# Kernel optimization log

Hardware: AMD Instinct MI355X
Metric: run time of the kernel (lower is better)

The kernel has to match this reference:

```python
import math
import jax, jax.numpy as jnp
import numpy as np

B, DIM, C, N = 1024, 512, 1000, 8
R = 0.05
WEIGHT_LAMBDA = 0.3
CN = C * N
TOPK = math.ceil(R * CN)  # 400


def setup_inputs() -> dict:
    key = jax.random.key(0)
    k1, k2, k3 = jax.random.split(key, 3)
    x = jax.random.normal(k1, (B, DIM), dtype=jnp.float32)
    # kaiming_uniform_(a=sqrt(5)) on a (DIM, CN) tensor: fan_in = CN (torch 2D fan_in = size(1)),
    # gain = sqrt(2/(1+a^2)) = sqrt(1/3), bound = gain * sqrt(3/fan_in)
    bound = math.sqrt(1.0 / 3.0) * math.sqrt(3.0 / CN)
    proxies = jax.random.uniform(k2, (DIM, CN), dtype=jnp.float32, minval=-bound, maxval=bound)
    target = jax.random.randint(k3, (B,), 0, C)
    return {"x": x, "proxies": proxies, "target": target}


def reference(x, proxies, target):
    instance_label = jnp.repeat(jnp.arange(C), N)  # (CN,)

    # F.normalize(Proxies, p=2, dim=0) with eps=1e-12 clamp
    norm = jnp.maximum(jnp.linalg.norm(proxies, axis=0, keepdims=True), 1e-12)
    centers = proxies / norm  # (DIM, CN)

    similarity = x @ centers  # (B, CN)

    positive_mask = (target[:, None] == instance_label[None, :]).astype(similarity.dtype)

    # topk over similarity boosted so all positives are included, then scatter 1s
    _, idx = jax.lax.top_k(similarity + 1000.0 * positive_mask, TOPK)  # (B, TOPK)
    mask = jnp.zeros_like(similarity).at[jnp.arange(B)[:, None], idx].set(1.0)
    mask = jax.lax.stop_gradient(mask)

    prob_a = mask * similarity  # (B, CN)
    # matmul with block one-hot y_instance_onehot == sum over the N proxies of each class
    logits = prob_a.reshape(B, C, N).sum(axis=-1)  # (B, C)

    logits_mask = jax.lax.stop_gradient((logits != 0.0).astype(logits.dtype))
    exp_l = jnp.exp(logits) * logits_mask
    predict = exp_l / (1e-8 + exp_l.sum(axis=1, keepdims=True))

    # sum(-y_onehot * log(predict+1e-20), 1) == -log(predict[b, target[b]] + 1e-20)
    loss_classify = jnp.mean(-jnp.log(predict[jnp.arange(B), target] + 1e-20))

    # regularizer: (centers.T @ centers) @ y_instance_onehot, fused as
    # centers.T @ (per-class sum of centers) -- identical math, avoids the CNxCN matrix
    centers_cls = centers.reshape(DIM, C, N).sum(axis=-1)  # (DIM, C)
    centers_logits = centers.T @ centers_cls  # (CN, C)
    logp = jax.nn.log_softmax(centers_logits, axis=1)
    reg = -jnp.mean(logp[jnp.arange(CN), instance_label])

    total = loss_classify + WEIGHT_LAMBDA * reg
    return (total, loss_classify)
```

## Files before the change

### kernel.cpp

```cpp
#include <hip/hip_runtime.h>
#include <hip/hip_bf16.h>
#include <math.h>

#define PB   1024
#define PDIM 512
#define PC   1000
#define PN   8
#define PCN  8000
#define PTOPK 400
#define NONPOS_K 392
#define NBIN 1024
#define CANDMAX 1024

typedef __bf16 bf16x8 __attribute__((ext_vector_type(8)));
typedef __bf16 bf16x4 __attribute__((ext_vector_type(4)));
typedef float  f32x4  __attribute__((ext_vector_type(4)));

__device__ static inline void async_load16(const __bf16* g, __bf16* l) {
    __builtin_amdgcn_global_load_lds(
        (const __attribute__((address_space(1))) void*)g,
        (__attribute__((address_space(3))) void*)l,
        16, 0, 0);
}

__global__ __launch_bounds__(256) void k_pre(const float* __restrict__ x,
                                             const float* __restrict__ P,
                                             __bf16* __restrict__ xb,
                                             float* __restrict__ ssqp,
                                             float* __restrict__ esd,
                                             float* __restrict__ padf,
                                             float* __restrict__ acc) {
    int b = blockIdx.x, tid = threadIdx.x;
    if (b == 0 && tid < 8) acc[tid] = 0.f;
    if (b < 512) {
        int i = b * 256 + tid;
        float4 v = ((const float4*)x)[i];
        bf16x4 o;
        o[0] = (__bf16)v.x; o[1] = (__bf16)v.y; o[2] = (__bf16)v.z; o[3] = (__bf16)v.w;
        ((bf16x4*)xb)[i] = o;
    } else if (b < 768) {
        int idx = b - 512;
        int slice = idx & 7, jb = idx >> 3;
        int j = jb * 256 + tid;
        if (j < PCN) {
            const float* p = P + (size_t)(slice * 64) * PCN + j;
            float ss = 0.f;
#pragma unroll 8
            for (int r = 0; r < 64; ++r) {
                float v = p[(size_t)r * PCN];
                ss = fmaf(v, v, ss);
            }
            ssqp[slice * PCN + j] = ss;
        }
    } else {
        int i = (b - 768) * 256 + tid;
        if (i < 16000) esd[i] = 0.f;
        else if (i < 16000 + 6144) padf[i - 16000] = 0.f;
    }
}

__global__ __launch_bounds__(256) void k_tpose(const float* __restrict__ P,
                                               const float* __restrict__ ssqp,
                                               __bf16* __restrict__ Pt,
                                               __bf16* __restrict__ ccls) {
    __shared__ float t[64][65];
    __shared__ float sinv[64];
    int tid = threadIdx.x;
    int tx = tid & 63, ty = tid >> 6;
    int j0 = blockIdx.x * 64, d0 = blockIdx.y * 64;
    if (tid < 64) {
        float sq = 0.f;
#pragma unroll
        for (int p2 = 0; p2 < 8; ++p2) sq += ssqp[p2 * PCN + j0 + tid];
        sinv[tid] = 1.0f / fmaxf(sqrtf(sq), 1e-12f);
    }
#pragma unroll
    for (int r = 0; r < 16; ++r) {
        int d = d0 + ty * 16 + r;
        t[ty * 16 + r][tx] = P[(size_t)d * PCN + j0 + tx];
    }
    __syncthreads();
    float cs0 = 0.f, cs1 = 0.f;
#pragma unroll
    for (int r = 0; r < 16; ++r) {
        int jl = ty * 16 + r;
        float val = t[tx][jl] * sinv[jl];
        Pt[(size_t)(j0 + jl) * PDIM + d0 + tx] = (__bf16)val;
        if (r < 8) cs0 += val; else cs1 += val;
    }
    int c0 = (j0 >> 3) + ty * 2;
    ccls[(size_t)c0 * PDIM + d0 + tx] = (__bf16)cs0;
    ccls[(size_t)(c0 + 1) * PDIM + d0 + tx] = (__bf16)cs1;
}

#define GEMM_STAGE(A, Bt, Ma, Nb, m0, n0, buf, k0) {                          \
    _Pragma("unroll")                                                         \
    for (int pass = 0; pass < 2; ++pass) {                                    \
        int cc_ = pass * 256 + w * 64 + lane;                                 \
        int arow = (m0) + (cc_ >> 2); if (arow > (Ma) - 1) arow = (Ma) - 1;   \
        async_load16((A) + (size_t)arow * PDIM + (k0) + (cc_ & 3) * 8,        \
                     &As[buf][cc_ * 8]);                                      \
        int brow = (n0) + (cc_ >> 2); if (brow > (Nb) - 1) brow = (Nb) - 1;   \
        async_load16((Bt) + (size_t)brow * PDIM + (k0) + (cc_ & 3) * 8,       \
                     &Bs[buf][cc_ * 8]);                                      \
    } }

#define GEMM_CORE(A, Bt, Ma, Nb, m0, n0)                                      \
    GEMM_STAGE(A, Bt, Ma, Nb, m0, n0, 0, 0)                                   \
    for (int it = 0; it < 16; ++it) {                                         \
        int cur = it & 1;                                                     \
        __syncthreads();                                                      \
        if (it < 15) GEMM_STAGE(A, Bt, Ma, Nb, m0, n0, cur ^ 1, (it + 1) * 32)\
        bf16x8 av[4], bv[4];                                                  \
        _Pragma("unroll")                                                     \
        for (int i = 0; i < 4; ++i) {                                         \
            av[i] = *(const bf16x8*)&As[cur][(wr * 64 + i * 16 + l15) * 32 + quad * 8]; \
            bv[i] = *(const bf16x8*)&Bs[cur][(wc * 64 + i * 16 + l15) * 32 + quad * 8]; \
        }                                                                     \
        _Pragma("unroll")                                                     \
        for (int i = 0; i < 4; ++i)                                           \
            _Pragma("unroll")                                                 \
            for (int j = 0; j < 4; ++j)                                       \
                acc[i][j] = __builtin_amdgcn_mfma_f32_16x16x32_bf16(          \
                    av[i], bv[j], acc[i][j], 0, 0, 0);                        \
    }

__global__ __launch_bounds__(256) void k_gemms(const __bf16* __restrict__ xb,
                                               const __bf16* __restrict__ Pt,
                                               const __bf16* __restrict__ ccls,
                                               __bf16* __restrict__ simb,
                                               float* __restrict__ esum,
                                               float* __restrict__ diag) {
    __shared__ __bf16 As[2][128 * 32];
    __shared__ __bf16 Bs[2][128 * 32];
    int tid = threadIdx.x;
    int w = tid >> 6, lane = tid & 63;
    int wr = w >> 1, wc = w & 1;
    int quad = lane >> 4, l15 = lane & 15;
    f32x4 acc[4][4] = {};
    int id = blockIdx.x;
    if (id < 504) {
        int n0 = (id % 63) * 128, m0 = (id / 63) * 128;
        GEMM_CORE(xb, Pt, PB, PCN, m0, n0)
#pragma unroll
        for (int i = 0; i < 4; ++i) {
            int r0 = m0 + wr * 64 + i * 16 + quad * 4;
#pragma unroll
            for (int j = 0; j < 4; ++j) {
                int cc = n0 + wc * 64 + j * 16 + l15;
                if (cc < PCN) {
#pragma unroll
                    for (int r = 0; r < 4; ++r)
                        simb[(size_t)(r0 + r) * PCN + cc] = (__bf16)acc[i][j][r];
                }
            }
        }
    } else {
        int id2 = id - 504;
        int n0 = (id2 % 8) * 128, m0 = (id2 / 8) * 128;
        GEMM_CORE(Pt, ccls, PCN, PB, m0, n0)
#pragma unroll
        for (int i = 0; i < 4; ++i) {
            int r0 = m0 + wr * 64 + i * 16 + quad * 4;
            float psum[4] = {0.f, 0.f, 0.f, 0.f};
#pragma unroll
            for (int j = 0; j < 4; ++j) {
                int cc = n0 + wc * 64 + j * 16 + l15;
                bool cvalid = (cc < PC);
#pragma unroll
                for (int r = 0; r < 4; ++r) {
                    float v = acc[i][j][r];
                    psum[r] += cvalid ? expf(v) : 0.f;
                    int rr = r0 + r;
                    if (cvalid && rr < PCN && cc == (rr >> 3)) diag[rr] = v;
                }
            }
#pragma unroll
            for (int off = 1; off < 16; off <<= 1)
#pragma unroll
                for (int r = 0; r < 4; ++r)
                    psum[r] += __shfl_xor(psum[r], off, 64);
            if (l15 == 0) {
#pragma unroll
                for (int r = 0; r < 4; ++r) {
                    int rr = r0 + r;
                    if (rr < PCN) atomicAdd(&esum[rr], psum[r]);
                }
            }
        }
    }
}

__global__ __launch_bounds__(256) void k_rowloss(const __bf16* __restrict__ sim,
                                                 const int* __restrict__ target,
                                                 float* __restrict__ acc) {
    __shared__ unsigned hist[NBIN];
    __shared__ float redf[8];
    __shared__ unsigned wtot[4];
    __shared__ float cand[CANDMAX];
    __shared__ unsigned candn;
    __shared__ int s_bin, s_A;
    __shared__ float s_tau;
    __shared__ int s_gt, s_eq;
    __shared__ float s_et;

    int b = blockIdx.x, tid = threadIdx.x;
    int lane = tid & 63, wv = tid >> 6;
    const bf16x8* row8 = (const bf16x8*)(sim + (size_t)b * PCN);
    int targ = target[b];

#pragma unroll
    for (int k = 0; k < 4; ++k) hist[tid + 256 * k] = 0u;
    if (tid == 0) candn = 0u;

    float pv[4][8];
    float lmn = INFINITY, lmx = -INFINITY;
#pragma unroll
    for (int k = 0; k < 4; ++k) {
        int c = tid + 256 * k;
        if (c < PC) {
            bf16x8 vv = row8[c];
#pragma unroll
            for (int n = 0; n < 8; ++n) pv[k][n] = (float)vv[n];
            if (c != targ) {
#pragma unroll
                for (int n = 0; n < 8; ++n) {
                    lmn = fminf(lmn, pv[k][n]);
                    lmx = fmaxf(lmx, pv[k][n]);
                }
            }
        } else {
#pragma unroll
            for (int n = 0; n < 8; ++n) pv[k][n] = 0.f;
        }
    }
    for (int off = 32; off; off >>= 1) {
        lmn = fminf(lmn, __shfl_down(lmn, off, 64));
        lmx = fmaxf(lmx, __shfl_down(lmx, off, 64));
    }
    if (lane == 0) { redf[wv] = lmn; redf[4 + wv] = lmx; }
    __syncthreads();
    float lo = fminf(fminf(redf[0], redf[1]), fminf(redf[2], redf[3]));
    float hi = fmaxf(fmaxf(redf[4], redf[5]), fmaxf(redf[6], redf[7]));
    float range = hi - lo;
    float scale = (range > 0.f) ? (float)NBIN / range : 0.f;

#pragma unroll
    for (int k = 0; k < 4; ++k) {
        int c = tid + 256 * k;
        if (c < PC && c != targ) {
#pragma unroll
            for (int n = 0; n < 8; ++n) {
                int bin = (int)((pv[k][n] - lo) * scale);
                bin = bin < 0 ? 0 : (bin > NBIN - 1 ? NBIN - 1 : bin);
                atomicAdd(&hist[bin], 1u);
            }
        }
    }
    __syncthreads();

    int b0 = tid * 4;
    unsigned h0 = hist[b0], h1 = hist[b0 + 1], h2 = hist[b0 + 2], h3 = hist[b0 + 3];
    unsigned l3 = h3, l2 = h2 + l3, l1 = h1 + l2, l0 = h0 + l1;
    unsigned T = l0;
#pragma unroll
    for (int step = 1; step < 64; step <<= 1) {
        unsigned u = __shfl_down(T, step, 64);
        if (lane + step < 64) T += u;
    }
    if (lane == 0) wtot[wv] = T;
    __syncthreads();
    unsigned tail = 0;
#pragma unroll
    for (int w2 = 0; w2 < 4; ++w2) if (w2 > wv) tail += wtot[w2];
    unsigned E = T - l0 + tail;
    {
        unsigned sfx[4] = {l0 + E, l1 + E, l2 + E, l3 + E};
        unsigned nxt[4] = {l1 + E, l2 + E, l3 + E, E};
#pragma unroll
        for (int i = 0; i < 4; ++i)
            if (sfx[i] >= NONPOS_K && nxt[i] < NONPOS_K) {
                s_bin = b0 + i;
                s_A = (int)nxt[i];
            }
    }
    __syncthreads();
    int tbin = s_bin, A = s_A;

#pragma unroll
    for (int k = 0; k < 4; ++k) {
        int c = tid + 256 * k;
        if (c < PC && c != targ) {
#pragma unroll
            for (int n = 0; n < 8; ++n) {
                int bin = (int)((pv[k][n] - lo) * scale);
                bin = bin < 0 ? 0 : (bin > NBIN - 1 ? NBIN - 1 : bin);
                if (bin == tbin) {
                    unsigned idx = atomicAdd(&candn, 1u);
                    if (idx < CANDMAX) cand[idx] = pv[k][n];
                }
            }
        }
    }
    __syncthreads();
    int m = (int)candn; if (m > CANDMAX) m = CANDMAX;
    int rank = NONPOS_K - A;
    for (int ci = tid; ci < m; ci += 256) {
        float val = cand[ci];
        int g = 0, e = 0;
        for (int i = 0; i < m; ++i) {
            g += cand[i] > val;
            e += cand[i] == val;
        }
        if (g < rank && rank <= g + e) { s_tau = val; s_gt = g; s_eq = e; }
    }
    __syncthreads();
    float tau = s_tau;
    int cgt = A + s_gt, ceq = s_eq;
    int rem = NONPOS_K - cgt;
    bool all_eq = (rem >= ceq);

    int offs[4] = {0, 0, 0, 0};
    if (!all_eq) {
        unsigned chunk_base = 0;
#pragma unroll
        for (int k = 0; k < 4; ++k) {
            int c = tid + 256 * k;
            unsigned tn = 0;
            if (c < PC && c != targ) {
#pragma unroll
                for (int n = 0; n < 8; ++n) tn += (pv[k][n] == tau) ? 1u : 0u;
            }
            unsigned inc = tn;
#pragma unroll
            for (int step = 1; step < 64; step <<= 1) {
                unsigned u = __shfl_up(inc, step, 64);
                if (lane >= step) inc += u;
            }
            __syncthreads();
            if (lane == 63) wtot[wv] = inc;
            __syncthreads();
            unsigned base = 0;
#pragma unroll
            for (int w2 = 0; w2 < 4; ++w2) if (w2 < wv) base += wtot[w2];
            offs[k] = (int)(chunk_base + base + inc - tn);
            chunk_base += wtot[0] + wtot[1] + wtot[2] + wtot[3];
        }
    }

    float psum = 0.f;
#pragma unroll
    for (int k = 0; k < 4; ++k) {
        int c = tid + 256 * k;
        if (c >= PC) continue;
        float lg = 0.f;
        if (c == targ) {
#pragma unroll
            for (int n = 0; n < 8; ++n) lg += pv[k][n];
        } else {
#pragma unroll
            for (int n = 0; n < 8; ++n) {
                float v = pv[k][n];
                bool sel = v > tau;
                if (!sel && v == tau) {
                    if (all_eq) sel = true;
                    else { sel = (offs[k] < rem); offs[k]++; }
                }
                if (sel) lg += v;
            }
        }
        float e = (lg != 0.0f) ? expf(lg) : 0.0f;
        psum += e;
        if (c == targ) s_et = e;
    }
    for (int off = 32; off; off >>= 1) psum += __shfl_down(psum, off, 64);
    if (lane == 0) redf[wv] = psum;
    __syncthreads();
    if (tid == 0) {
        float denom = 1e-8f + redf[0] + redf[1] + redf[2] + redf[3];
        atomicAdd(acc, -logf(s_et / denom + 1e-20f));
    }
}

__global__ __launch_bounds__(256) void k_final(const float* __restrict__ esum,
                                               const float* __restrict__ diag,
                                               const float* __restrict__ acc,
                                               float* __restrict__ out) {
    __shared__ float redf[4];
    int tid = threadIdx.x, lane = tid & 63, wv = tid >> 6;
    float s = 0.f;
    for (int j = tid; j < PCN; j += 256)
        s += logf(esum[j]) - diag[j];
    for (int off = 32; off; off >>= 1) s += __shfl_down(s, off, 64);
    if (lane == 0) redf[wv] = s;
    __syncthreads();
    if (tid == 0) {
        float rg = (redf[0] + redf[1] + redf[2] + redf[3]) * (1.0f / PCN);
        float lc = acc[0] * (1.0f / PB);
        out[0] = lc + 0.3f * rg;
        out[1] = lc;
    }
}

extern "C" void kernel_launch(void* const* d_in, const int* in_sizes, int n_in,
                              void* d_out, int out_size, void* d_ws, size_t ws_size,
                              hipStream_t stream) {
    const float* x       = (const float*)d_in[0];
    const float* proxies = (const float*)d_in[1];
    const int*   target  = (const int*)d_in[2];
    float* out = (float*)d_out;
    float* ws  = (float*)d_ws;

    float*  acc   = ws;
    float*  ssqp  = ws + 64;
    float*  esum  = ws + 64064;
    float*  diag  = ws + 72064;
    __bf16* xb    = (__bf16*)(ws + 80064);
    __bf16* cclsb = (__bf16*)(ws + 342208);
    __bf16* Pt    = (__bf16*)(ws + 604352);
    __bf16* simb  = (__bf16*)(ws + 2652352);

    float* padf = (float*)cclsb + 256000;

    k_pre<<<856, 256, 0, stream>>>(x, proxies, xb, ssqp, esum, padf, acc);
    k_tpose<<<dim3(125, 8), 256, 0, stream>>>(proxies, ssqp, Pt, cclsb);

    k_gemms<<<1008, 256, 0, stream>>>(xb, Pt, cclsb, simb, esum, diag);

    k_rowloss<<<PB, 256, 0, stream>>>(simb, target, acc);
    k_final<<<1, 256, 0, stream>>>(esum, diag, acc, out);
}
```

Baseline: 146.3 us.

## Use 32x32 MFMA tiles and exact two-pass radix select on bf16 keys

The GEMM inner loop moves from 16x16x32 to 32x32x16 bf16 MFMA with a 2x2 tile per wave, and the epilogues are rewritten for the new accumulator layout. The row-loss top-k threshold search replaces the min/max float histogram plus quadratic candidate ranking with an exact two-level radix histogram (high byte, then low byte) on order-preserving 16-bit bf16 keys, using per-wave sub-histograms to reduce shared atomic contention. This removes the O(m^2) candidate scan and the float bin arithmetic. The costs are more shuffles and atomics in the regularizer epilogue and a different MFMA register layout.

```diff
diff --git a/kernel.cpp b/kernel.cpp
--- a/kernel.cpp
+++ b/kernel.cpp
@@ -9,12 +9,10 @@
 #define PCN  8000
 #define PTOPK 400
 #define NONPOS_K 392
-#define NBIN 1024
-#define CANDMAX 1024
 
 typedef __bf16 bf16x8 __attribute__((ext_vector_type(8)));
 typedef __bf16 bf16x4 __attribute__((ext_vector_type(4)));
-typedef float  f32x4  __attribute__((ext_vector_type(4)));
+typedef float  f32x16 __attribute__((ext_vector_type(16)));
 
 __device__ static inline void async_load16(const __bf16* g, __bf16* l) {
     __builtin_amdgcn_global_load_lds(
@@ -111,18 +109,21 @@
         int cur = it & 1;                                                     \
         __syncthreads();                                                      \
         if (it < 15) GEMM_STAGE(A, Bt, Ma, Nb, m0, n0, cur ^ 1, (it + 1) * 32)\
-        bf16x8 av[4], bv[4];                                                  \
         _Pragma("unroll")                                                     \
-        for (int i = 0; i < 4; ++i) {                                         \
-            av[i] = *(const bf16x8*)&As[cur][(wr * 64 + i * 16 + l15) * 32 + quad * 8]; \
-            bv[i] = *(const bf16x8*)&Bs[cur][(wc * 64 + i * 16 + l15) * 32 + quad * 8]; \
+        for (int h = 0; h < 2; ++h) {                                         \
+            bf16x8 av[2], bv[2];                                              \
+            _Pragma("unroll")                                                 \
+            for (int t2 = 0; t2 < 2; ++t2) {                                  \
+                av[t2] = *(const bf16x8*)&As[cur][(wr * 64 + t2 * 32 + l31) * 32 + h * 16 + half8]; \
+                bv[t2] = *(const bf16x8*)&Bs[cur][(wc * 64 + t2 * 32 + l31) * 32 + h * 16 + half8]; \
+            }                                                                 \
+            _Pragma("unroll")                                                 \
+            for (int ti = 0; ti < 2; ++ti)                                    \
+                _Pragma("unroll")                                             \
+                for (int tj = 0; tj < 2; ++tj)                                \
+                    acc[ti][tj] = __builtin_amdgcn_mfma_f32_32x32x16_bf16(    \
+                        av[ti], bv[tj], acc[ti][tj], 0, 0, 0);                \
         }                                                                     \
-        _Pragma("unroll")                                                     \
-        for (int i = 0; i < 4; ++i)                                           \
-            _Pragma("unroll")                                                 \
-            for (int j = 0; j < 4; ++j)                                       \
-                acc[i][j] = __builtin_amdgcn_mfma_f32_16x16x32_bf16(          \
-                    av[i], bv[j], acc[i][j], 0, 0, 0);                        \
     }
 
 __global__ __launch_bounds__(256) void k_gemms(const __bf16* __restrict__ xb,
@@ -136,55 +137,57 @@
     int tid = threadIdx.x;
     int w = tid >> 6, lane = tid & 63;
     int wr = w >> 1, wc = w & 1;
-    int quad = lane >> 4, l15 = lane & 15;
-    f32x4 acc[4][4] = {};
+    int l31 = lane & 31, half8 = (lane >> 5) * 8;
+    f32x16 acc[2][2] = {};
     int id = blockIdx.x;
     if (id < 504) {
         int n0 = (id % 63) * 128, m0 = (id / 63) * 128;
         GEMM_CORE(xb, Pt, PB, PCN, m0, n0)
 #pragma unroll
-        for (int i = 0; i < 4; ++i) {
-            int r0 = m0 + wr * 64 + i * 16 + quad * 4;
-#pragma unroll
-            for (int j = 0; j < 4; ++j) {
-                int cc = n0 + wc * 64 + j * 16 + l15;
+        for (int ti = 0; ti < 2; ++ti)
+#pragma unroll
+            for (int tj = 0; tj < 2; ++tj) {
+                int cc = n0 + wc * 64 + tj * 32 + l31;
                 if (cc < PCN) {
 #pragma unroll
-                    for (int r = 0; r < 4; ++r)
-                        simb[(size_t)(r0 + r) * PCN + cc] = (__bf16)acc[i][j][r];
+                    for (int reg = 0; reg < 16; ++reg) {
+                        int rr = m0 + wr * 64 + ti * 32
+                               + (reg & 3) + 8 * (reg >> 2) + 4 * (lane >> 5);
+                        simb[(size_t)rr * PCN + cc] = (__bf16)acc[ti][tj][reg];
+                    }
                 }
             }
-        }
     } else {
         int id2 = id - 504;
         int n0 = (id2 % 8) * 128, m0 = (id2 / 8) * 128;
         GEMM_CORE(Pt, ccls, PCN, PB, m0, n0)
 #pragma unroll
-        for (int i = 0; i < 4; ++i) {
-            int r0 = m0 + wr * 64 + i * 16 + quad * 4;
-            float psum[4] = {0.f, 0.f, 0.f, 0.f};
-#pragma unroll
-            for (int j = 0; j < 4; ++j) {
-                int cc = n0 + wc * 64 + j * 16 + l15;
+        for (int ti = 0; ti < 2; ++ti) {
+            float ps[16] = {};
+#pragma unroll
+            for (int tj = 0; tj < 2; ++tj) {
+                int cc = n0 + wc * 64 + tj * 32 + l31;
                 bool cvalid = (cc < PC);
 #pragma unroll
-                for (int r = 0; r < 4; ++r) {
-                    float v = acc[i][j][r];
-                    psum[r] += cvalid ? expf(v) : 0.f;
-                    int rr = r0 + r;
-                    if (cvalid && rr < PCN && cc == (rr >> 3)) diag[rr] = v;
+                for (int reg = 0; reg < 16; ++reg) {
+                    float v = acc[ti][tj][reg];
+                    int rr = m0 + wr * 64 + ti * 32
+                           + (reg & 3) + 8 * (reg >> 2) + 4 * (lane >> 5);
+                    if (cvalid) {
+                        ps[reg] += expf(v);
+                        if (rr < PCN && cc == (rr >> 3)) diag[rr] = v;
+                    }
                 }
             }
 #pragma unroll
-            for (int off = 1; off < 16; off <<= 1)
-#pragma unroll
-                for (int r = 0; r < 4; ++r)
-                    psum[r] += __shfl_xor(psum[r], off, 64);
-            if (l15 == 0) {
-#pragma unroll
-                for (int r = 0; r < 4; ++r) {
-                    int rr = r0 + r;
-                    if (rr < PCN) atomicAdd(&esum[rr], psum[r]);
+            for (int reg = 0; reg < 16; ++reg) {
+#pragma unroll
+                for (int off = 1; off < 32; off <<= 1)
+                    ps[reg] += __shfl_xor(ps[reg], off, 64);
+                if (l31 == 0) {
+                    int rr = m0 + wr * 64 + ti * 32
+                           + (reg & 3) + 8 * (reg >> 2) + 4 * (lane >> 5);
+                    if (rr < PCN) atomicAdd(&esum[rr], ps[reg]);
                 }
             }
         }
@@ -194,98 +197,68 @@
 __global__ __launch_bounds__(256) void k_rowloss(const __bf16* __restrict__ sim,
                                                  const int* __restrict__ target,
                                                  float* __restrict__ acc) {
-    __shared__ unsigned hist[NBIN];
-    __shared__ float redf[8];
+    __shared__ unsigned hist[4][256];
     __shared__ unsigned wtot[4];
-    __shared__ float cand[CANDMAX];
-    __shared__ unsigned candn;
-    __shared__ int s_bin, s_A;
-    __shared__ float s_tau;
-    __shared__ int s_gt, s_eq;
+    __shared__ float redf[4];
+    __shared__ int s_hb, s_A1, s_lb, s_A2, s_eq;
     __shared__ float s_et;
 
     int b = blockIdx.x, tid = threadIdx.x;
     int lane = tid & 63, wv = tid >> 6;
-    const bf16x8* row8 = (const bf16x8*)(sim + (size_t)b * PCN);
+    const uint4* row16 = (const uint4*)(sim + (size_t)b * PCN);
     int targ = target[b];
 
 #pragma unroll
-    for (int k = 0; k < 4; ++k) hist[tid + 256 * k] = 0u;
-    if (tid == 0) candn = 0u;
-
-    float pv[4][8];
-    float lmn = INFINITY, lmx = -INFINITY;
+    for (int k = 0; k < 4; ++k) hist[k][tid] = 0u;
+
+    uint4 kv[4];
 #pragma unroll
     for (int k = 0; k < 4; ++k) {
         int c = tid + 256 * k;
-        if (c < PC) {
-            bf16x8 vv = row8[c];
-#pragma unroll
-            for (int n = 0; n < 8; ++n) pv[k][n] = (float)vv[n];
-            if (c != targ) {
-#pragma unroll
-                for (int n = 0; n < 8; ++n) {
-                    lmn = fminf(lmn, pv[k][n]);
-                    lmx = fmaxf(lmx, pv[k][n]);
-                }
-            }
-        } else {
-#pragma unroll
-            for (int n = 0; n < 8; ++n) pv[k][n] = 0.f;
-        }
-    }
-    for (int off = 32; off; off >>= 1) {
-        lmn = fminf(lmn, __shfl_down(lmn, off, 64));
-        lmx = fmaxf(lmx, __shfl_down(lmx, off, 64));
-    }
-    if (lane == 0) { redf[wv] = lmn; redf[4 + wv] = lmx; }
-    __syncthreads();
-    float lo = fminf(fminf(redf[0], redf[1]), fminf(redf[2], redf[3]));
-    float hi = fmaxf(fmaxf(redf[4], redf[5]), fmaxf(redf[6], redf[7]));
-    float range = hi - lo;
-    float scale = (range > 0.f) ? (float)NBIN / range : 0.f;
+        kv[k] = (c < PC) ? row16[c] : make_uint4(0u, 0u, 0u, 0u);
+    }
+    __syncthreads();
+
+#define KEYOF(k, n) ({                                                        \
+    unsigned u_ = ((const unsigned*)&kv[k])[(n) >> 1];                        \
+    unsigned c_ = ((n) & 1) ? (u_ >> 16) : (u_ & 0xFFFFu);                    \
+    (c_ & 0x8000u) ? (c_ ^ 0xFFFFu) : (c_ | 0x8000u); })
+#define VALOF(k, n) ({                                                        \
+    unsigned u_ = ((const unsigned*)&kv[k])[(n) >> 1];                        \
+    unsigned c_ = ((n) & 1) ? (u_ & 0xFFFF0000u) : (u_ << 16);                \
+    __uint_as_float(c_); })
 
 #pragma unroll
     for (int k = 0; k < 4; ++k) {
         int c = tid + 256 * k;
         if (c < PC && c != targ) {
 #pragma unroll
-            for (int n = 0; n < 8; ++n) {
-                int bin = (int)((pv[k][n] - lo) * scale);
-                bin = bin < 0 ? 0 : (bin > NBIN - 1 ? NBIN - 1 : bin);
-                atomicAdd(&hist[bin], 1u);
-            }
-        }
-    }
-    __syncthreads();
-
-    int b0 = tid * 4;
-    unsigned h0 = hist[b0], h1 = hist[b0 + 1], h2 = hist[b0 + 2], h3 = hist[b0 + 3];
-    unsigned l3 = h3, l2 = h2 + l3, l1 = h1 + l2, l0 = h0 + l1;
-    unsigned T = l0;
-#pragma unroll
-    for (int step = 1; step < 64; step <<= 1) {
-        unsigned u = __shfl_down(T, step, 64);
-        if (lane + step < 64) T += u;
-    }
-    if (lane == 0) wtot[wv] = T;
-    __syncthreads();
-    unsigned tail = 0;
-#pragma unroll
-    for (int w2 = 0; w2 < 4; ++w2) if (w2 > wv) tail += wtot[w2];
-    unsigned E = T - l0 + tail;
+            for (int n = 0; n < 8; ++n)
+                atomicAdd(&hist[wv][KEYOF(k, n) >> 8], 1u);
+        }
+    }
+    __syncthreads();
+
+    unsigned h1 = hist[0][tid] + hist[1][tid] + hist[2][tid] + hist[3][tid];
     {
-        unsigned sfx[4] = {l0 + E, l1 + E, l2 + E, l3 + E};
-        unsigned nxt[4] = {l1 + E, l2 + E, l3 + E, E};
-#pragma unroll
-        for (int i = 0; i < 4; ++i)
-            if (sfx[i] >= NONPOS_K && nxt[i] < NONPOS_K) {
-                s_bin = b0 + i;
-                s_A = (int)nxt[i];
-            }
-    }
-    __syncthreads();
-    int tbin = s_bin, A = s_A;
+        unsigned inc = h1;
+#pragma unroll
+        for (int step = 1; step < 64; step <<= 1) {
+            unsigned u = __shfl_down(inc, step, 64);
+            if (lane + step < 64) inc += u;
+        }
+        if (lane == 0) wtot[wv] = inc;
+        __syncthreads();
+        unsigned tail = 0;
+#pragma unroll
+        for (int w2 = 0; w2 < 4; ++w2) if (w2 > wv) tail += wtot[w2];
+        unsigned sfx = inc + tail, nxt = sfx - h1;
+        if (sfx >= NONPOS_K && nxt < NONPOS_K) { s_hb = tid; s_A1 = (int)nxt; }
+    }
+    __syncthreads();
+    int hb = s_hb, A1 = s_A1;
+    hist[0][tid] = 0u;
+    __syncthreads();
 
 #pragma unroll
     for (int k = 0; k < 4; ++k) {
@@ -293,30 +266,35 @@
         if (c < PC && c != targ) {
 #pragma unroll
             for (int n = 0; n < 8; ++n) {
-                int bin = (int)((pv[k][n] - lo) * scale);
-                bin = bin < 0 ? 0 : (bin > NBIN - 1 ? NBIN - 1 : bin);
-                if (bin == tbin) {
-                    unsigned idx = atomicAdd(&candn, 1u);
-                    if (idx < CANDMAX) cand[idx] = pv[k][n];
-                }
-            }
-        }
-    }
-    __syncthreads();
-    int m = (int)candn; if (m > CANDMAX) m = CANDMAX;
-    int rank = NONPOS_K - A;
-    for (int ci = tid; ci < m; ci += 256) {
-        float val = cand[ci];
-        int g = 0, e = 0;
-        for (int i = 0; i < m; ++i) {
-            g += cand[i] > val;
-            e += cand[i] == val;
-        }
-        if (g < rank && rank <= g + e) { s_tau = val; s_gt = g; s_eq = e; }
-    }
-    __syncthreads();
-    float tau = s_tau;
-    int cgt = A + s_gt, ceq = s_eq;
+                unsigned key = KEYOF(k, n);
+                if ((int)(key >> 8) == hb) atomicAdd(&hist[0][key & 255u], 1u);
+            }
+        }
+    }
+    __syncthreads();
+    unsigned h2 = hist[0][tid];
+    {
+        int rank2 = NONPOS_K - A1;
+        unsigned inc = h2;
+#pragma unroll
+        for (int step = 1; step < 64; step <<= 1) {
+            unsigned u = __shfl_down(inc, step, 64);
+            if (lane + step < 64) inc += u;
+        }
+        __syncthreads();
+        if (lane == 0) wtot[wv] = inc;
+        __syncthreads();
+        unsigned tail = 0;
+#pragma unroll
+        for (int w2 = 0; w2 < 4; ++w2) if (w2 > wv) tail += wtot[w2];
+        unsigned sfx = inc + tail, nxt = sfx - h2;
+        if (sfx >= (unsigned)rank2 && nxt < (unsigned)rank2) {
+            s_lb = tid; s_A2 = (int)nxt; s_eq = (int)h2;
+        }
+    }
+    __syncthreads();
+    unsigned tkey = ((unsigned)hb << 8) | (unsigned)s_lb;
+    int cgt = A1 + s_A2, ceq = s_eq;
     int rem = NONPOS_K - cgt;
     bool all_eq = (rem >= ceq);
 
@@ -329,7 +307,7 @@
             unsigned tn = 0;
             if (c < PC && c != targ) {
 #pragma unroll
-                for (int n = 0; n < 8; ++n) tn += (pv[k][n] == tau) ? 1u : 0u;
+                for (int n = 0; n < 8; ++n) tn += (KEYOF(k, n) == tkey) ? 1u : 0u;
             }
             unsigned inc = tn;
 #pragma unroll
@@ -356,17 +334,17 @@
         float lg = 0.f;
         if (c == targ) {
 #pragma unroll
-            for (int n = 0; n < 8; ++n) lg += pv[k][n];
+            for (int n = 0; n < 8; ++n) lg += VALOF(k, n);
         } else {
 #pragma unroll
             for (int n = 0; n < 8; ++n) {
-                float v = pv[k][n];
-                bool sel = v > tau;
-                if (!sel && v == tau) {
+                unsigned key = KEYOF(k, n);
+                bool sel = key > tkey;
+                if (!sel && key == tkey) {
                     if (all_eq) sel = true;
                     else { sel = (offs[k] < rem); offs[k]++; }
                 }
-                if (sel) lg += v;
+                if (sel) lg += VALOF(k, n);
             }
         }
         float e = (lg != 0.0f) ? expf(lg) : 0.0f;
@@ -380,6 +358,8 @@
         float denom = 1e-8f + redf[0] + redf[1] + redf[2] + redf[3];
         atomicAdd(acc, -logf(s_et / denom + 1e-20f));
     }
+#undef KEYOF
+#undef VALOF
 }
 
 __global__ __launch_bounds__(256) void k_final(const float* __restrict__ esum,
```

Measured after the change: 163.6 us. 11.8% more time.
